# Kernel optimization log

Measured on AMD Instinct MI355X. Metric: run time of the kernel, lower is better.

## Reference

```python
import jax, jax.numpy as jnp
import numpy as np

D_MODEL = 1024
N_HEAD = 16
HEAD_DIM = D_MODEL // N_HEAD
B, T = 4, 1024
MIN_KEEP_H, MAX_KEEP_H = 2, 6


def setup_inputs() -> dict:
    key = jax.random.key(0)
    ks = jax.random.split(key, 8)
    x = jax.random.normal(ks[0], (B, T, D_MODEL), dtype=jnp.float32)
    # SignMaskLinear weight: uniform(-1, 1)
    q_w = jax.random.uniform(ks[1], (D_MODEL, D_MODEL), minval=-1.0, maxval=1.0, dtype=jnp.float32)
    # BitGhostLinear weights: randn
    k_w = jax.random.normal(ks[2], (D_MODEL, D_MODEL), dtype=jnp.float32)
    v_w = jax.random.normal(ks[3], (D_MODEL, D_MODEL), dtype=jnp.float32)
    o_w = jax.random.normal(ks[4], (D_MODEL, D_MODEL), dtype=jnp.float32)
    zeros = jnp.zeros((D_MODEL,), dtype=jnp.float32)
    return {"x": x, "q_w": q_w, "q_b": zeros, "k_w": k_w, "k_b": zeros,
            "v_w": v_w, "v_b": zeros, "o_w": o_w, "o_b": zeros}


def _ghost_attention(x, q_w, q_b, k_w, k_b, v_w, v_b, o_w, o_b):
    Bn, Tn, C = x.shape
    H, Dh = N_HEAD, HEAD_DIM
    # SignMaskLinear: effective weight is sign(w) * (w != 0)
    qw_eff = jnp.sign(q_w) * (q_w != 0).astype(x.dtype)
    q = (x @ qw_eff.T + q_b).reshape(Bn, Tn, H, Dh).transpose(0, 2, 1, 3)  # (B,H,T,Dh)
    k = (x @ k_w.T + k_b).reshape(Bn, Tn, H, Dh).transpose(0, 2, 1, 3)
    v = (x @ v_w.T + v_b).reshape(Bn, Tn, H, Dh).transpose(0, 2, 1, 3)
    # RMS-normalize q
    q = q / (jnp.sqrt(jnp.mean(q * q, axis=-1, keepdims=True)) + 1e-6)
    # Per-head top-k sparsification of q by |q| (static keep counts)
    ratios = np.linspace(0.35, 0.15, H)
    keep_counts = np.maximum((ratios * Dh).astype(np.int64), 1)  # trunc like .long()
    q_abs = jnp.abs(q)
    q_sorted = -jnp.sort(-q_abs, axis=-1)  # descending along Dh
    idx = jnp.asarray(keep_counts - 1, dtype=jnp.int32).reshape(1, H, 1, 1)
    thresh = jnp.take_along_axis(q_sorted, jnp.broadcast_to(idx, (Bn, H, Tn, 1)), axis=-1)
    q = q * (q_abs >= thresh).astype(q.dtype)
    # RMS-normalize k
    k = k / (jnp.sqrt(jnp.mean(k * k, axis=-1, keepdims=True)) + 1e-6)
    # Causal masked attention (no scale factor in original)
    logits = jnp.einsum('bhqd,bhkd->bhqk', q, k)
    causal = jnp.tril(jnp.ones((Tn, Tn), dtype=bool))
    logits = jnp.where(causal[None, None], logits, -jnp.inf)
    attn = jax.nn.softmax(logits, axis=-1)
    # Entropy-driven adaptive head pruning
    head_energy = jnp.mean(attn ** 2, axis=(2, 3))  # (B,H)
    head_prob = jax.nn.softmax(head_energy, axis=1)
    head_entropy = -jnp.sum(head_prob * jnp.log(head_prob + 1e-9), axis=1)  # (B,)
    ent_norm = jnp.clip(head_entropy / jnp.log(jnp.float32(H)), 0.0, 1.0)
    keep_h = jnp.round(MIN_KEEP_H + ent_norm * (MAX_KEEP_H - MIN_KEEP_H)).astype(jnp.int32)  # (B,)
    he_sorted = -jnp.sort(-head_energy, axis=1)  # descending (B,H)
    thresh_h = jnp.take_along_axis(he_sorted, (keep_h - 1)[:, None], axis=1)  # (B,1)
    head_mask = (head_energy >= thresh_h).astype(x.dtype)[:, :, None, None]  # (B,H,1,1)
    attn = attn * head_mask
    v = v * head_mask
    out = jnp.einsum('bhqk,bhkd->bhqd', attn, v).transpose(0, 2, 1, 3).reshape(Bn, Tn, C)
    return out @ o_w.T + o_b


def reference(x, q_w, q_b, k_w, k_b, v_w, v_b, o_w, o_b):
    return _ghost_attention(x, q_w, q_b, k_w, k_b, v_w, v_b, o_w, o_b)
```

## Files before the change

kernel.cpp:

```cpp
#include <hip/hip_runtime.h>
#include <math.h>

#define D_MODEL 1024
#define T_SEQ   1024
#define BATCH   4
#define NHEAD   16
#define HDIM    64

__constant__ int KEEPC[16] = {22,21,20,19,18,18,17,16,15,14,13,13,12,11,10,9};

typedef short bh8  __attribute__((ext_vector_type(8)));
typedef float f32x4 __attribute__((ext_vector_type(4)));
typedef int   i32x4 __attribute__((ext_vector_type(4)));

__device__ __forceinline__ unsigned short f2bf(float f) {
    unsigned int u = __float_as_uint(f);
    return (unsigned short)((u + 0x7FFFu + ((u >> 16) & 1u)) >> 16);
}
__device__ __forceinline__ float bf2f(unsigned short h) {
    return __uint_as_float(((unsigned int)h) << 16);
}

__global__ void cast_prep(const float* __restrict__ kw,
                          unsigned short* __restrict__ kwh,
                          unsigned short* __restrict__ kwl,
                          const float* __restrict__ vw,
                          unsigned short* __restrict__ vwb,
                          const float* __restrict__ ow,
                          unsigned short* __restrict__ owb,
                          const float* __restrict__ x,
                          signed char* __restrict__ dig,
                          const float* __restrict__ qw,
                          signed char* __restrict__ sg)
{
    const int NS = (D_MODEL * D_MODEL) / 8;
    const int NX = (BATCH * T_SEQ * D_MODEL) / 8;
    int i = blockIdx.x * 256 + threadIdx.x;

    if (i < 3 * NS) {
        const float* src; unsigned short* dh; unsigned short* dl = nullptr;
        long off;
        if (i < NS)          { src = kw; dh = kwh; dl = kwl; off = i; }
        else if (i < 2 * NS) { src = vw; dh = vwb; off = i - NS; }
        else                 { src = ow; dh = owb; off = i - 2 * NS; }
        long e = off * 8;
        alignas(16) float fl[8];
        *(float4*)&fl[0] = *(const float4*)(src + e);
        *(float4*)&fl[4] = *(const float4*)(src + e + 4);
        uint4 hp, lp;
        unsigned int* hpw = (unsigned int*)&hp;
        unsigned int* lpw = (unsigned int*)&lp;
        #pragma unroll
        for (int c = 0; c < 4; c++) {
            unsigned short h0 = f2bf(fl[2 * c]), h1 = f2bf(fl[2 * c + 1]);
            hpw[c] = (unsigned int)h0 | ((unsigned int)h1 << 16);
            if (dl) {
                unsigned short l0 = f2bf(fl[2 * c] - bf2f(h0));
                unsigned short l1 = f2bf(fl[2 * c + 1] - bf2f(h1));
                lpw[c] = (unsigned int)l0 | ((unsigned int)l1 << 16);
            }
        }
        *(uint4*)(dh + e) = hp;
        if (dl) *(uint4*)(dl + e) = lp;
    } else if (i < 3 * NS + NX) {
        long e = (long)(i - 3 * NS) * 8;
        alignas(16) float f[8];
        *(float4*)&f[0] = *(const float4*)(x + e);
        *(float4*)&f[4] = *(const float4*)(x + e + 4);
        signed char d[4][8];
        #pragma unroll
        for (int c = 0; c < 8; c++) {
            int n = (int)rintf(f[c] * 8388608.0f);
            int d0 = (signed char)(n & 0xff); n = (n - d0) >> 8;
            int d1 = (signed char)(n & 0xff); n = (n - d1) >> 8;
            int d2 = (signed char)(n & 0xff); n = (n - d2) >> 8;
            d[0][c] = (signed char)d0; d[1][c] = (signed char)d1;
            d[2][c] = (signed char)d2; d[3][c] = (signed char)n;
        }
        long row = e >> 10;
        int  kk  = (int)(e & 1023);
        long rt  = row >> 4;
        int  l15r = (int)(row & 15);
        int  kstep = kk >> 6;
        int  rg2 = (kk >> 4) & 3;
        int  L = rg2 * 16 + l15r;
        int  t = kk & 15;
        signed char* dp = dig + (rt << 16) + ((long)kstep << 12)
                              + ((long)L << 4) + t;
        #pragma unroll
        for (int p = 0; p < 4; p++)
            *(uint2*)(dp + (p << 10)) = *(uint2*)&d[p][0];
    } else if (i < 3 * NS + NX + NS) {
        long e = (long)(i - 3 * NS - NX) * 8;
        alignas(16) float f[8];
        *(float4*)&f[0] = *(const float4*)(qw + e);
        *(float4*)&f[4] = *(const float4*)(qw + e + 4);
        signed char s[8];
        #pragma unroll
        for (int c = 0; c < 8; c++)
            s[c] = (signed char)((f[c] > 0.f) - (f[c] < 0.f));
        long col = e >> 10;
        int  kk  = (int)(e & 1023);
        long ct  = col >> 4;
        int  l15c = (int)(col & 15);
        int  kstep = kk >> 6;
        int  rg2 = (kk >> 4) & 3;
        int  L = rg2 * 16 + l15c;
        int  t = kk & 15;
        signed char* sp = sg + (ct << 14) + ((long)kstep << 10)
                             + ((long)L << 4) + t;
        *(uint2*)sp = *(uint2*)&s[0];
    }
}

__global__ __launch_bounds__(256, 4) void gemm_q_i8(
    const signed char* __restrict__ dig, const signed char* __restrict__ sg,
    const float* __restrict__ Bi, unsigned short* __restrict__ Yq)
{
    int tid  = threadIdx.x;
    int blk  = blockIdx.x;
    int low  = blk & 7, rest = blk >> 3;
    int bn   = (rest & 15) * 64;
    int bm   = (((rest >> 4) << 3) + low) * 64;
    int wave = tid >> 6, lane = tid & 63;
    int l15  = lane & 15, rg = lane >> 4;

    int rt  = (bm >> 4) + wave;
    int ct0 = bn >> 4;

    i32x4 acc[4][4];
    #pragma unroll
    for (int p = 0; p < 4; p++)
        #pragma unroll
        for (int j = 0; j < 4; j++) acc[p][j] = (i32x4)0;

    const signed char* ar = dig + ((size_t)rt << 16) + (lane << 4);
    const signed char* br = sg + ((size_t)ct0 << 14) + (lane << 4);

    i32x4 aA[4], bA[4], aB[4], bB[4];
    #pragma unroll
    for (int p = 0; p < 4; p++) aA[p] = *(const i32x4*)(ar + (p << 10));
    #pragma unroll
    for (int j = 0; j < 4; j++) bA[j] = *(const i32x4*)(br + (j << 14));

    #pragma unroll
    for (int kk = 0; kk < 8; kk++) {
        #pragma unroll
        for (int p = 0; p < 4; p++) aB[p] = *(const i32x4*)(ar + 4096 + (p << 10));
        #pragma unroll
        for (int j = 0; j < 4; j++) bB[j] = *(const i32x4*)(br + 1024 + (j << 14));
        #pragma unroll
        for (int p = 0; p < 4; p++)
            #pragma unroll
            for (int j = 0; j < 4; j++)
                acc[p][j] = __builtin_amdgcn_mfma_i32_16x16x64_i8(
                    aA[p], bA[j], acc[p][j], 0, 0, 0);
        if (kk < 7) {
            #pragma unroll
            for (int p = 0; p < 4; p++) aA[p] = *(const i32x4*)(ar + 8192 + (p << 10));
            #pragma unroll
            for (int j = 0; j < 4; j++) bA[j] = *(const i32x4*)(br + 2048 + (j << 14));
        }
        #pragma unroll
        for (int p = 0; p < 4; p++)
            #pragma unroll
            for (int j = 0; j < 4; j++)
                acc[p][j] = __builtin_amdgcn_mfma_i32_16x16x64_i8(
                    aB[p], bB[j], acc[p][j], 0, 0, 0);
        ar += 8192; br += 2048;
    }

    int hh   = bn >> 6;
    int keep = KEEPC[hh];
    float bvj[4];
    #pragma unroll
    for (int j = 0; j < 4; j++) bvj[j] = Bi[bn + j * 16 + l15];

    float xv[4][4];
    #pragma unroll
    for (int j = 0; j < 4; j++)
        #pragma unroll
        for (int r = 0; r < 4; r++) {
            long t = (long)acc[0][j][r]
                   + ((long)acc[1][j][r] << 8)
                   + ((long)acc[2][j][r] << 16)
                   + ((long)acc[3][j][r] << 24);
            xv[j][r] = (float)((double)t * (1.0 / 8388608.0)) + bvj[j];
        }

    unsigned int shiftv = (unsigned int)(rg & 1) * 16;
    #pragma unroll
    for (int r = 0; r < 4; r++) {
        float ss = xv[0][r] * xv[0][r] + xv[1][r] * xv[1][r]
                 + xv[2][r] * xv[2][r] + xv[3][r] * xv[3][r];
        ss += __shfl_xor(ss, 1); ss += __shfl_xor(ss, 2);
        ss += __shfl_xor(ss, 4); ss += __shfl_xor(ss, 8);
        float rms = sqrtf(ss * (1.0f / 64.0f));

        float xn[4]; unsigned int ai[4];
        #pragma unroll
        for (int j = 0; j < 4; j++) {
            xn[j] = xv[j][r] / (rms + 1e-6f);
            ai[j] = __float_as_uint(fabsf(xn[j]));
        }

        unsigned int th = 0;
        for (int bit = 30; bit >= 0; --bit) {
            unsigned int cand = th | (1u << bit);
            int cnt = 0;
            #pragma unroll
            for (int j = 0; j < 4; j++) {
                unsigned long long bl = __ballot(ai[j] >= cand);
                unsigned int half = (rg & 2) ? (unsigned int)(bl >> 32)
                                             : (unsigned int)bl;
                cnt += __popc((half >> shiftv) & 0xFFFFu);
            }
            if (cnt >= keep) th = cand;
        }

        int row = bm + wave * 16 + rg * 4 + r;
        int bb = row >> 10, tt = row & 1023;
        unsigned int* qp32 = (unsigned int*)(Yq
            + (((size_t)(bb * NHEAD + hh)) * T_SEQ + tt) * 128);
        #pragma unroll
        for (int j = 0; j < 4; j++) {
            float o = (ai[j] < th) ? 0.f : xn[j];
            unsigned short hi = f2bf(o);
            unsigned short lo = f2bf(o - bf2f(hi));
            qp32[j * 16 + l15] = (unsigned int)hi | ((unsigned int)lo << 16);
        }
    }
}

#define GLDK 72

__global__ __launch_bounds__(256, 2) void gemm_kv(
    const float* __restrict__ A,
    const unsigned short* __restrict__ kwh, const unsigned short* __restrict__ kwl,
    const float* __restrict__ kb,
    const unsigned short* __restrict__ vwb, const float* __restrict__ vb,
    unsigned short* __restrict__ Yk, unsigned short* __restrict__ Yv)
{
    __shared__ unsigned short Ah[128 * GLDK];
    __shared__ unsigned short Al[128 * GLDK];
    __shared__ unsigned short Whs[128 * GLDK];
    __shared__ unsigned short Wls[128 * GLDK];

    int tid  = threadIdx.x;
    int blk  = blockIdx.x;
    int z    = blk >> 8;
    int split = (z == 0);
    int inner = blk & 255;
    int low  = inner & 7, rest = inner >> 3;
    int bn   = (rest & 7) * 128;
    int bm   = (((rest >> 3) << 3) + low) * 128;
    const unsigned short* Wh = split ? kwh : vwb;
    const unsigned short* Wl = split ? kwl : vwb;
    const float*          Bi = split ? kb : vb;

    int wave = tid >> 6, lane = tid & 63;
    int l15  = lane & 15, q4 = lane >> 4;
    int wm   = (wave >> 1) * 64, wn = (wave & 1) * 64;
    int srow = tid >> 1;
    int scol = (tid & 1) * 32;

    f32x4 acc[4][4];
    #pragma unroll
    for (int i = 0; i < 4; i++)
        #pragma unroll
        for (int j = 0; j < 4; j++) acc[i][j] = (f32x4)0.f;

    const float* ap = A + (size_t)(bm + srow) * D_MODEL + scol;
    const unsigned short* whp = Wh + (size_t)(bn + srow) * D_MODEL + scol;
    const unsigned short* wlp = Wl + (size_t)(bn + srow) * D_MODEL + scol;

    for (int k0 = 0; k0 < D_MODEL; k0 += 64) {
        alignas(16) float fl[32];
        #pragma unroll
        for (int c = 0; c < 8; c++) *(float4*)&fl[4 * c] = *(const float4*)(ap + 4 * c);
        uint4 w0 = *(const uint4*)(whp + 0),  w1 = *(const uint4*)(whp + 8);
        uint4 w2 = *(const uint4*)(whp + 16), w3 = *(const uint4*)(whp + 24);
        uint4 x0, x1, x2, x3;
        if (split) {
            x0 = *(const uint4*)(wlp + 0);  x1 = *(const uint4*)(wlp + 8);
            x2 = *(const uint4*)(wlp + 16); x3 = *(const uint4*)(wlp + 24);
        }
        ap += 64; whp += 64; wlp += 64;

        unsigned int hw[16], lw[16];
        #pragma unroll
        for (int c = 0; c < 16; c++) {
            unsigned short h0 = f2bf(fl[2 * c]), h1 = f2bf(fl[2 * c + 1]);
            hw[c] = (unsigned int)h0 | ((unsigned int)h1 << 16);
            if (split) {
                unsigned short l0 = f2bf(fl[2 * c] - bf2f(h0));
                unsigned short l1 = f2bf(fl[2 * c + 1] - bf2f(h1));
                lw[c] = (unsigned int)l0 | ((unsigned int)l1 << 16);
            }
        }

        __syncthreads();
        unsigned int* ah = (unsigned int*)&Ah[srow * GLDK + scol];
        #pragma unroll
        for (int g = 0; g < 4; g++)
            *(uint4*)(ah + 4 * g) = make_uint4(hw[4 * g], hw[4 * g + 1], hw[4 * g + 2], hw[4 * g + 3]);
        if (split) {
            unsigned int* al = (unsigned int*)&Al[srow * GLDK + scol];
            #pragma unroll
            for (int g = 0; g < 4; g++)
                *(uint4*)(al + 4 * g) = make_uint4(lw[4 * g], lw[4 * g + 1], lw[4 * g + 2], lw[4 * g + 3]);
        }
        unsigned short* ws = &Whs[srow * GLDK + scol];
        *(uint4*)(ws + 0) = w0; *(uint4*)(ws + 8)  = w1;
        *(uint4*)(ws + 16) = w2; *(uint4*)(ws + 24) = w3;
        if (split) {
            unsigned short* wl2 = &Wls[srow * GLDK + scol];
            *(uint4*)(wl2 + 0) = x0; *(uint4*)(wl2 + 8)  = x1;
            *(uint4*)(wl2 + 16) = x2; *(uint4*)(wl2 + 24) = x3;
        }
        __syncthreads();

        #pragma unroll
        for (int kc = 0; kc < 64; kc += 32) {
            bh8 ahf[4], whf[4];
            #pragma unroll
            for (int i = 0; i < 4; i++)
                ahf[i] = *(bh8*)&Ah[(wm + i * 16 + l15) * GLDK + kc + q4 * 8];
            #pragma unroll
            for (int j = 0; j < 4; j++)
                whf[j] = *(bh8*)&Whs[(wn + j * 16 + l15) * GLDK + kc + q4 * 8];
            #pragma unroll
            for (int i = 0; i < 4; i++)
                #pragma unroll
                for (int j = 0; j < 4; j++)
                    acc[i][j] = __builtin_amdgcn_mfma_f32_16x16x32_bf16(ahf[i], whf[j], acc[i][j], 0, 0, 0);
            if (split) {
                bh8 alf[4], wlf[4];
                #pragma unroll
                for (int i = 0; i < 4; i++)
                    alf[i] = *(bh8*)&Al[(wm + i * 16 + l15) * GLDK + kc + q4 * 8];
                #pragma unroll
                for (int j = 0; j < 4; j++)
                    wlf[j] = *(bh8*)&Wls[(wn + j * 16 + l15) * GLDK + kc + q4 * 8];
                #pragma unroll
                for (int i = 0; i < 4; i++)
                    #pragma unroll
                    for (int j = 0; j < 4; j++) {
                        acc[i][j] = __builtin_amdgcn_mfma_f32_16x16x32_bf16(ahf[i], wlf[j], acc[i][j], 0, 0, 0);
                        acc[i][j] = __builtin_amdgcn_mfma_f32_16x16x32_bf16(alf[i], whf[j], acc[i][j], 0, 0, 0);
                    }
            }
        }
    }

    if (split) {
        int hh = (bn + wn) >> 6;
        float bv[4];
        #pragma unroll
        for (int j = 0; j < 4; j++) bv[j] = Bi[bn + wn + j * 16 + l15];
        #pragma unroll
        for (int i = 0; i < 4; i++) {
            #pragma unroll
            for (int r = 0; r < 4; r++) {
                int row = bm + wm + i * 16 + q4 * 4 + r;
                int bb = row >> 10, tt = row & 1023;
                float vv[4]; float ss = 0.f;
                #pragma unroll
                for (int j = 0; j < 4; j++) {
                    vv[j] = acc[i][j][r] + bv[j];
                    ss += vv[j] * vv[j];
                }
                ss += __shfl_xor(ss, 1); ss += __shfl_xor(ss, 2);
                ss += __shfl_xor(ss, 4); ss += __shfl_xor(ss, 8);
                float rms = sqrtf(ss * (1.0f / 64.0f));
                unsigned short* kp = Yk + (((size_t)(bb * NHEAD + hh)) * T_SEQ + tt) * 128;
                #pragma unroll
                for (int j = 0; j < 4; j++) {
                    float xn = vv[j] / (rms + 1e-6f);
                    unsigned short hi = f2bf(xn);
                    unsigned short lo = f2bf(xn - bf2f(hi));
                    kp[j * 16 + l15]      = hi;
                    kp[64 + j * 16 + l15] = lo;
                }
            }
        }
    } else {
        #pragma unroll
        for (int j = 0; j < 4; j++) {
            int col = bn + wn + j * 16 + l15;
            int hh = col >> 6, dd = col & 63;
            float bvv = Bi[col];
            #pragma unroll
            for (int i = 0; i < 4; i++) {
                int row0 = bm + wm + i * 16 + q4 * 4;
                int bb = row0 >> 10, tt = row0 & 1023;
                uint2 u;
                u.x = (unsigned int)f2bf(acc[i][j][0] + bvv) | ((unsigned int)f2bf(acc[i][j][1] + bvv) << 16);
                u.y = (unsigned int)f2bf(acc[i][j][2] + bvv) | ((unsigned int)f2bf(acc[i][j][3] + bvv) << 16);
                *(uint2*)(Yv + ((size_t)(bb * NHEAD + hh) * HDIM + dd) * T_SEQ + tt) = u;
            }
        }
    }
}

#define KST 72

__global__ __launch_bounds__(256, 4) void attn_kernel(
    const unsigned short* __restrict__ Qsg,
    const unsigned short* __restrict__ Ksg,
    const unsigned short* __restrict__ Vtg,
    unsigned short* __restrict__ Ctx, double* __restrict__ He)
{
    __shared__ unsigned short Kh[64 * KST];
    __shared__ unsigned short Kl[64 * KST];
    __shared__ unsigned short Vt[64 * KST];
    __shared__ unsigned short Ps[4][16 * KST];

    int tid = threadIdx.x;
    int blk = blockIdx.x;
    int low = blk & 7, rest = blk >> 3;
    int qt  = 15 - (rest & 15);
    int r2  = rest >> 4;
    int h   = (r2 & 1) * 8 + low;
    int b   = r2 >> 1;
    int bh = b * NHEAD + h;
    size_t rbase = (size_t)bh * T_SEQ;

    int wave = tid >> 6, lane = tid & 63;
    int l15 = lane & 15, rg = lane >> 4;
    int srow = tid >> 2;
    int scol = (tid & 3) * 16;

    int qrow = qt * 64 + wave * 16 + l15;

    bh8 qf[2][2];
    {
        const unsigned int* qp32 = (const unsigned int*)(Qsg + (rbase + qrow) * 128);
        uint4 a = *(const uint4*)(qp32 + rg * 8);
        uint4 c = *(const uint4*)(qp32 + rg * 8 + 4);
        uint4 d = *(const uint4*)(qp32 + 32 + rg * 8);
        uint4 e = *(const uint4*)(qp32 + 32 + rg * 8 + 4);
        unsigned int hv[4], lv[4];
        hv[0] = __builtin_amdgcn_perm(a.y, a.x, 0x05040100u);
        hv[1] = __builtin_amdgcn_perm(a.w, a.z, 0x05040100u);
        hv[2] = __builtin_amdgcn_perm(c.y, c.x, 0x05040100u);
        hv[3] = __builtin_amdgcn_perm(c.w, c.z, 0x05040100u);
        lv[0] = __builtin_amdgcn_perm(a.y, a.x, 0x07060302u);
        lv[1] = __builtin_amdgcn_perm(a.w, a.z, 0x07060302u);
        lv[2] = __builtin_amdgcn_perm(c.y, c.x, 0x07060302u);
        lv[3] = __builtin_amdgcn_perm(c.w, c.z, 0x07060302u);
        qf[0][0] = *(bh8*)hv;
        qf[1][0] = *(bh8*)lv;
        hv[0] = __builtin_amdgcn_perm(d.y, d.x, 0x05040100u);
        hv[1] = __builtin_amdgcn_perm(d.w, d.z, 0x05040100u);
        hv[2] = __builtin_amdgcn_perm(e.y, e.x, 0x05040100u);
        hv[3] = __builtin_amdgcn_perm(e.w, e.z, 0x05040100u);
        lv[0] = __builtin_amdgcn_perm(d.y, d.x, 0x07060302u);
        lv[1] = __builtin_amdgcn_perm(d.w, d.z, 0x07060302u);
        lv[2] = __builtin_amdgcn_perm(e.y, e.x, 0x07060302u);
        lv[3] = __builtin_amdgcn_perm(e.w, e.z, 0x07060302u);
        qf[0][1] = *(bh8*)hv;
        qf[1][1] = *(bh8*)lv;
    }

    float m = -1e30f, l = 0.f, s2 = 0.f;
    f32x4 o[4];
    #pragma unroll
    for (int n = 0; n < 4; n++) o[n] = (f32x4)0.f;

    unsigned short* myPs = &Ps[wave][0];
    const unsigned short* vbase = Vtg + (size_t)bh * HDIM * T_SEQ;

    for (int kt = 0; kt <= qt; ++kt) {
        const unsigned short* krow = Ksg + (rbase + kt * 64 + srow) * 128;
        uint4 kh0 = *(const uint4*)(krow + scol);
        uint4 kh1 = *(const uint4*)(krow + scol + 8);
        uint4 kl0 = *(const uint4*)(krow + 64 + scol);
        uint4 kl1 = *(const uint4*)(krow + 64 + scol + 8);
        const unsigned short* vrow = vbase + (size_t)srow * T_SEQ + kt * 64 + scol;
        uint4 vv0 = *(const uint4*)(vrow);
        uint4 vv1 = *(const uint4*)(vrow + 8);

        __syncthreads();
        *(uint4*)&Kh[srow * KST + scol]     = kh0;
        *(uint4*)&Kh[srow * KST + scol + 8] = kh1;
        *(uint4*)&Kl[srow * KST + scol]     = kl0;
        *(uint4*)&Kl[srow * KST + scol + 8] = kl1;
        *(uint4*)&Vt[srow * KST + scol]     = vv0;
        *(uint4*)&Vt[srow * KST + scol + 8] = vv1;
        __syncthreads();

        f32x4 s[4];
        #pragma unroll
        for (int n = 0; n < 4; n++) s[n] = (f32x4)0.f;
        #pragma unroll
        for (int n = 0; n < 4; n++) {
            const unsigned short* kr = &Kh[(n * 16 + l15) * KST + rg * 8];
            const unsigned short* lr = &Kl[(n * 16 + l15) * KST + rg * 8];
            bh8 ah0 = *(const bh8*)(kr);
            bh8 ah1 = *(const bh8*)(kr + 32);
            bh8 al0 = *(const bh8*)(lr);
            bh8 al1 = *(const bh8*)(lr + 32);
            s[n] = __builtin_amdgcn_mfma_f32_16x16x32_bf16(ah0, qf[0][0], s[n], 0, 0, 0);
            s[n] = __builtin_amdgcn_mfma_f32_16x16x32_bf16(ah1, qf[0][1], s[n], 0, 0, 0);
            s[n] = __builtin_amdgcn_mfma_f32_16x16x32_bf16(ah0, qf[1][0], s[n], 0, 0, 0);
            s[n] = __builtin_amdgcn_mfma_f32_16x16x32_bf16(ah1, qf[1][1], s[n], 0, 0, 0);
            s[n] = __builtin_amdgcn_mfma_f32_16x16x32_bf16(al0, qf[0][0], s[n], 0, 0, 0);
            s[n] = __builtin_amdgcn_mfma_f32_16x16x32_bf16(al1, qf[0][1], s[n], 0, 0, 0);
        }

        if (kt == qt) {
            #pragma unroll
            for (int n = 0; n < 4; n++)
                #pragma unroll
                for (int e2 = 0; e2 < 4; e2++)
                    if (n * 16 + rg * 4 + e2 > wave * 16 + l15) s[n][e2] = -1e30f;
        }

        float mx = -1e30f;
        #pragma unroll
        for (int n = 0; n < 4; n++)
            #pragma unroll
            for (int e2 = 0; e2 < 4; e2++) mx = fmaxf(mx, s[n][e2]);
        mx = fmaxf(mx, __shfl_xor(mx, 16));
        mx = fmaxf(mx, __shfl_xor(mx, 32));
        float mn = fmaxf(m, mx);
        float alpha = __expf(m - mn);
        m = mn;
        float rs = 0.f, rs2 = 0.f;
        #pragma unroll
        for (int n = 0; n < 4; n++)
            #pragma unroll
            for (int e2 = 0; e2 < 4; e2++) {
                float pv = __expf(s[n][e2] - mn);
                s[n][e2] = pv;
                rs += pv; rs2 += pv * pv;
            }
        rs  += __shfl_xor(rs, 16);  rs  += __shfl_xor(rs, 32);
        rs2 += __shfl_xor(rs2, 16); rs2 += __shfl_xor(rs2, 32);
        l  = l * alpha + rs;
        s2 = s2 * alpha * alpha + rs2;

        #pragma unroll
        for (int n = 0; n < 4; n++) {
            uint2 u;
            u.x = (unsigned int)f2bf(s[n][0]) | ((unsigned int)f2bf(s[n][1]) << 16);
            u.y = (unsigned int)f2bf(s[n][2]) | ((unsigned int)f2bf(s[n][3]) << 16);
            *(uint2*)&myPs[l15 * KST + n * 16 + rg * 4] = u;
        }
        bh8 pf0 = *(bh8*)&myPs[l15 * KST + rg * 8];
        bh8 pf1 = *(bh8*)&myPs[l15 * KST + 32 + rg * 8];

        #pragma unroll
        for (int n = 0; n < 4; n++) {
            o[n] *= alpha;
            const unsigned short* vr = &Vt[(n * 16 + l15) * KST + rg * 8];
            bh8 v0 = *(const bh8*)(vr);
            bh8 v1 = *(const bh8*)(vr + 32);
            o[n] = __builtin_amdgcn_mfma_f32_16x16x32_bf16(v0, pf0, o[n], 0, 0, 0);
            o[n] = __builtin_amdgcn_mfma_f32_16x16x32_bf16(v1, pf1, o[n], 0, 0, 0);
        }
    }

    float linv = 1.f / l;
    float en = (rg == 0) ? s2 * linv * linv : 0.f;
    en += __shfl_xor(en, 1); en += __shfl_xor(en, 2);
    en += __shfl_xor(en, 4); en += __shfl_xor(en, 8);
    if (lane == 0) atomicAdd(&He[bh], (double)en);

    unsigned short* cp = Ctx + ((size_t)b * T_SEQ + qrow) * D_MODEL + h * HDIM;
    #pragma unroll
    for (int n = 0; n < 4; n++) {
        uint2 u;
        u.x = (unsigned int)f2bf(o[n][0] * linv) | ((unsigned int)f2bf(o[n][1] * linv) << 16);
        u.y = (unsigned int)f2bf(o[n][2] * linv) | ((unsigned int)f2bf(o[n][3] * linv) << 16);
        *(uint2*)(cp + n * 16 + rg * 4) = u;
    }
}

__global__ __launch_bounds__(256, 2) void gemm_obf(
    const unsigned short* __restrict__ A, const unsigned short* __restrict__ W,
    const float* __restrict__ Bi, float* __restrict__ Y,
    const double* __restrict__ He)
{
    __shared__ unsigned short As[128 * GLDK];
    __shared__ unsigned short Ws[128 * GLDK];
    __shared__ double hs[34];
    __shared__ float maskS[NHEAD];

    int tid  = threadIdx.x;
    int blk  = blockIdx.x;
    int low  = blk & 7, rest = blk >> 3;
    int bn   = (rest & 7) * 128;
    int bm   = (((rest >> 3) << 3) + low) * 128;
    int batch = bm >> 10;

    if (tid < NHEAD) hs[tid] = He[batch * NHEAD + tid] * (1.0 / (1024.0 * 1024.0));
    __syncthreads();
    if (tid < NHEAD) {
        double mx = hs[0];
        for (int h2 = 1; h2 < NHEAD; h2++) mx = fmax(mx, hs[h2]);
        hs[NHEAD + tid] = exp(hs[tid] - mx);
    }
    __syncthreads();
    if (tid == 0) {
        double s = 0.0;
        for (int h2 = 0; h2 < NHEAD; h2++) s += hs[NHEAD + h2];
        hs[32] = s;
    }
    __syncthreads();
    if (tid < NHEAD) {
        double ph = hs[NHEAD + tid] / hs[32];
        hs[NHEAD + tid] = ph * log(ph + 1e-9);
    }
    __syncthreads();
    if (tid == 0) {
        double ent = 0.0;
        for (int h2 = 0; h2 < NHEAD; h2++) ent -= hs[NHEAD + h2];
        double entn = ent / log(16.0);
        entn = fmin(fmax(entn, 0.0), 1.0);
        int keep = (int)rint(2.0 + entn * 4.0);
        if (keep < 1) keep = 1;
        if (keep > NHEAD) keep = NHEAD;
        double srt[NHEAD];
        for (int h2 = 0; h2 < NHEAD; h2++) srt[h2] = hs[h2];
        for (int i = 1; i < NHEAD; i++) {
            double v = srt[i]; int j = i - 1;
            while (j >= 0 && srt[j] < v) { srt[j + 1] = srt[j]; j--; }
            srt[j + 1] = v;
        }
        double th = srt[keep - 1];
        for (int h2 = 0; h2 < NHEAD; h2++)
            maskS[h2] = (hs[h2] >= th) ? 1.0f : 0.0f;
    }
    __syncthreads();

    int wave = tid >> 6, lane = tid & 63;
    int l15  = lane & 15, q4 = lane >> 4;
    int wm   = (wave >> 1) * 64, wn = (wave & 1) * 64;
    int srow = tid >> 1;
    int scol = (tid & 1) * 32;

    f32x4 acc[4][4];
    #pragma unroll
    for (int i = 0; i < 4; i++)
        #pragma unroll
        for (int j = 0; j < 4; j++) acc[i][j] = (f32x4)0.f;

    const unsigned short* ap = A + (size_t)(bm + srow) * D_MODEL + scol;
    const unsigned short* wp = W + (size_t)(bn + srow) * D_MODEL + scol;

    for (int k0 = 0; k0 < D_MODEL; k0 += 64) {
        if (maskS[k0 >> 6] == 0.f) { ap += 64; wp += 64; continue; }

        uint4 a0 = *(const uint4*)(ap + 0),  a1 = *(const uint4*)(ap + 8);
        uint4 a2 = *(const uint4*)(ap + 16), a3 = *(const uint4*)(ap + 24);
        uint4 w0 = *(const uint4*)(wp + 0),  w1 = *(const uint4*)(wp + 8);
        uint4 w2 = *(const uint4*)(wp + 16), w3 = *(const uint4*)(wp + 24);
        ap += 64; wp += 64;
        __syncthreads();
        unsigned short* as = &As[srow * GLDK + scol];
        *(uint4*)(as + 0) = a0; *(uint4*)(as + 8)  = a1;
        *(uint4*)(as + 16) = a2; *(uint4*)(as + 24) = a3;
        unsigned short* ws = &Ws[srow * GLDK + scol];
        *(uint4*)(ws + 0) = w0; *(uint4*)(ws + 8)  = w1;
        *(uint4*)(ws + 16) = w2; *(uint4*)(ws + 24) = w3;
        __syncthreads();

        #pragma unroll
        for (int kc = 0; kc < 64; kc += 32) {
            bh8 af[4], wf[4];
            #pragma unroll
            for (int i = 0; i < 4; i++)
                af[i] = *(bh8*)&As[(wm + i * 16 + l15) * GLDK + kc + q4 * 8];
            #pragma unroll
            for (int j = 0; j < 4; j++)
                wf[j] = *(bh8*)&Ws[(wn + j * 16 + l15) * GLDK + kc + q4 * 8];
            #pragma unroll
            for (int i = 0; i < 4; i++)
                #pragma unroll
                for (int j = 0; j < 4; j++)
                    acc[i][j] = __builtin_amdgcn_mfma_f32_16x16x32_bf16(af[i], wf[j], acc[i][j], 0, 0, 0);
        }
    }

    #pragma unroll
    for (int j = 0; j < 4; j++) {
        int col = bn + wn + j * 16 + l15;
        float bv = Bi[col];
        #pragma unroll
        for (int i = 0; i < 4; i++) {
            int row = bm + wm + i * 16 + q4 * 4;
            #pragma unroll
            for (int r = 0; r < 4; r++)
                Y[(size_t)(row + r) * D_MODEL + col] = acc[i][j][r] + bv;
        }
    }
}

extern "C" void kernel_launch(void* const* d_in, const int* in_sizes, int n_in,
                              void* d_out, int out_size, void* d_ws, size_t ws_size,
                              hipStream_t stream)
{
    (void)in_sizes; (void)n_in; (void)out_size; (void)ws_size;
    const float* x  = (const float*)d_in[0];
    const float* qw = (const float*)d_in[1];
    const float* qb = (const float*)d_in[2];
    const float* kw = (const float*)d_in[3];
    const float* kb = (const float*)d_in[4];
    const float* vw = (const float*)d_in[5];
    const float* vb = (const float*)d_in[6];
    const float* ow = (const float*)d_in[7];
    const float* ob = (const float*)d_in[8];
    float* out = (float*)d_out;

    char* base = (char*)d_ws;
    const size_t MB = (size_t)1024 * 1024;
    unsigned short* qbf  = (unsigned short*)(base);
    unsigned short* kbf  = (unsigned short*)(base + 16 * MB);
    unsigned short* vt   = (unsigned short*)(base + 32 * MB);
    unsigned short* ctxb = (unsigned short*)(base + 40 * MB);
    signed char*    dig  = (signed char*)(base + 32 * MB);
    unsigned short* kwh  = (unsigned short*)(base + 48 * MB);
    unsigned short* kwl  = (unsigned short*)(base + 50 * MB);
    unsigned short* vwb  = (unsigned short*)(base + 52 * MB);
    unsigned short* owb  = (unsigned short*)(base + 54 * MB);
    signed char*    sg   = (signed char*)(base + 56 * MB);
    double*         he   = (double*)(base + 57 * MB);

    hipMemsetAsync(he, 0, 64 * sizeof(double), stream);

    cast_prep<<<4096, 256, 0, stream>>>(kw, kwh, kwl, vw, vwb, ow, owb,
                                        x, dig, qw, sg);
    gemm_q_i8<<<1024, 256, 0, stream>>>(dig, sg, qb, qbf);
    gemm_kv<<<512, 256, 0, stream>>>(x, kwh, kwl, kb, vwb, vb, kbf, vt);
    attn_kernel<<<1024, 256, 0, stream>>>(qbf, kbf, vt, ctxb, he);
    gemm_obf<<<256, 256, 0, stream>>>(ctxb, owb, ob, out, he);
}
```

Baseline: 279.5 us.

## Precompute x bf16 hi/lo split in prep and prefetch next K-tile in gemm_kv

The cast_prep kernel now also writes bf16 hi and lo copies of x, so gemm_kv loads pre-split bf16 instead of fp32 and no longer redoes the split conversion in every tile block. gemm_kv also moves to register prefetching: the next K-slice's global loads are issued after the shared-memory store and before the MFMA compute. This is meant to remove redundant conversion ALU work and hide global load latency. It costs an extra 16MB write in prep plus more live registers, which may affect occupancy under launch_bounds(256,2).

Measured after the change: 256.3 us (median of 2 runs). 1.09x faster.

```diff
diff --git a/kernel.cpp b/kernel.cpp
--- a/kernel.cpp
+++ b/kernel.cpp
@@ -30,6 +30,8 @@
                           unsigned short* __restrict__ owb,
                           const float* __restrict__ x,
                           signed char* __restrict__ dig,
+                          unsigned short* __restrict__ xh,
+                          unsigned short* __restrict__ xl,
                           const float* __restrict__ qw,
                           signed char* __restrict__ sg)
 {
@@ -90,6 +92,19 @@
         #pragma unroll
         for (int p = 0; p < 4; p++)
             *(uint2*)(dp + (p << 10)) = *(uint2*)&d[p][0];
+        uint4 hp, lp;
+        unsigned int* hpw = (unsigned int*)&hp;
+        unsigned int* lpw = (unsigned int*)&lp;
+        #pragma unroll
+        for (int c = 0; c < 4; c++) {
+            unsigned short h0 = f2bf(f[2 * c]), h1 = f2bf(f[2 * c + 1]);
+            hpw[c] = (unsigned int)h0 | ((unsigned int)h1 << 16);
+            unsigned short l0 = f2bf(f[2 * c] - bf2f(h0));
+            unsigned short l1 = f2bf(f[2 * c + 1] - bf2f(h1));
+            lpw[c] = (unsigned int)l0 | ((unsigned int)l1 << 16);
+        }
+        *(uint4*)(xh + e) = hp;
+        *(uint4*)(xl + e) = lp;
     } else if (i < 3 * NS + NX + NS) {
         long e = (long)(i - 3 * NS - NX) * 8;
         alignas(16) float f[8];
@@ -235,7 +250,7 @@
 #define GLDK 72
 
 __global__ __launch_bounds__(256, 2) void gemm_kv(
-    const float* __restrict__ A,
+    const unsigned short* __restrict__ xhg, const unsigned short* __restrict__ xlg,
     const unsigned short* __restrict__ kwh, const unsigned short* __restrict__ kwl,
     const float* __restrict__ kb,
     const unsigned short* __restrict__ vwb, const float* __restrict__ vb,
@@ -270,55 +285,55 @@
         #pragma unroll
         for (int j = 0; j < 4; j++) acc[i][j] = (f32x4)0.f;
 
-    const float* ap = A + (size_t)(bm + srow) * D_MODEL + scol;
+    const unsigned short* ahp = xhg + (size_t)(bm + srow) * D_MODEL + scol;
+    const unsigned short* alp = xlg + (size_t)(bm + srow) * D_MODEL + scol;
     const unsigned short* whp = Wh + (size_t)(bn + srow) * D_MODEL + scol;
     const unsigned short* wlp = Wl + (size_t)(bn + srow) * D_MODEL + scol;
 
+    uint4 a0, a1, a2, a3, g0, g1, g2, g3;
+    uint4 w0, w1, w2, w3, x0, x1, x2, x3;
+    a0 = *(const uint4*)(ahp + 0);  a1 = *(const uint4*)(ahp + 8);
+    a2 = *(const uint4*)(ahp + 16); a3 = *(const uint4*)(ahp + 24);
+    w0 = *(const uint4*)(whp + 0);  w1 = *(const uint4*)(whp + 8);
+    w2 = *(const uint4*)(whp + 16); w3 = *(const uint4*)(whp + 24);
+    if (split) {
+        g0 = *(const uint4*)(alp + 0);  g1 = *(const uint4*)(alp + 8);
+        g2 = *(const uint4*)(alp + 16); g3 = *(const uint4*)(alp + 24);
+        x0 = *(const uint4*)(wlp + 0);  x1 = *(const uint4*)(wlp + 8);
+        x2 = *(const uint4*)(wlp + 16); x3 = *(const uint4*)(wlp + 24);
+    }
+
     for (int k0 = 0; k0 < D_MODEL; k0 += 64) {
-        alignas(16) float fl[32];
-        #pragma unroll
-        for (int c = 0; c < 8; c++) *(float4*)&fl[4 * c] = *(const float4*)(ap + 4 * c);
-        uint4 w0 = *(const uint4*)(whp + 0),  w1 = *(const uint4*)(whp + 8);
-        uint4 w2 = *(const uint4*)(whp + 16), w3 = *(const uint4*)(whp + 24);
-        uint4 x0, x1, x2, x3;
-        if (split) {
-            x0 = *(const uint4*)(wlp + 0);  x1 = *(const uint4*)(wlp + 8);
-            x2 = *(const uint4*)(wlp + 16); x3 = *(const uint4*)(wlp + 24);
-        }
-        ap += 64; whp += 64; wlp += 64;
-
-        unsigned int hw[16], lw[16];
-        #pragma unroll
-        for (int c = 0; c < 16; c++) {
-            unsigned short h0 = f2bf(fl[2 * c]), h1 = f2bf(fl[2 * c + 1]);
-            hw[c] = (unsigned int)h0 | ((unsigned int)h1 << 16);
-            if (split) {
-                unsigned short l0 = f2bf(fl[2 * c] - bf2f(h0));
-                unsigned short l1 = f2bf(fl[2 * c + 1] - bf2f(h1));
-                lw[c] = (unsigned int)l0 | ((unsigned int)l1 << 16);
-            }
-        }
-
         __syncthreads();
-        unsigned int* ah = (unsigned int*)&Ah[srow * GLDK + scol];
-        #pragma unroll
-        for (int g = 0; g < 4; g++)
-            *(uint4*)(ah + 4 * g) = make_uint4(hw[4 * g], hw[4 * g + 1], hw[4 * g + 2], hw[4 * g + 3]);
-        if (split) {
-            unsigned int* al = (unsigned int*)&Al[srow * GLDK + scol];
-            #pragma unroll
-            for (int g = 0; g < 4; g++)
-                *(uint4*)(al + 4 * g) = make_uint4(lw[4 * g], lw[4 * g + 1], lw[4 * g + 2], lw[4 * g + 3]);
-        }
+        unsigned short* as = &Ah[srow * GLDK + scol];
+        *(uint4*)(as + 0) = a0; *(uint4*)(as + 8)  = a1;
+        *(uint4*)(as + 16) = a2; *(uint4*)(as + 24) = a3;
         unsigned short* ws = &Whs[srow * GLDK + scol];
         *(uint4*)(ws + 0) = w0; *(uint4*)(ws + 8)  = w1;
         *(uint4*)(ws + 16) = w2; *(uint4*)(ws + 24) = w3;
         if (split) {
+            unsigned short* als = &Al[srow * GLDK + scol];
+            *(uint4*)(als + 0) = g0; *(uint4*)(als + 8)  = g1;
+            *(uint4*)(als + 16) = g2; *(uint4*)(als + 24) = g3;
             unsigned short* wl2 = &Wls[srow * GLDK + scol];
             *(uint4*)(wl2 + 0) = x0; *(uint4*)(wl2 + 8)  = x1;
             *(uint4*)(wl2 + 16) = x2; *(uint4*)(wl2 + 24) = x3;
         }
         __syncthreads();
+
+        if (k0 + 64 < D_MODEL) {
+            ahp += 64; alp += 64; whp += 64; wlp += 64;
+            a0 = *(const uint4*)(ahp + 0);  a1 = *(const uint4*)(ahp + 8);
+            a2 = *(const uint4*)(ahp + 16); a3 = *(const uint4*)(ahp + 24);
+            w0 = *(const uint4*)(whp + 0);  w1 = *(const uint4*)(whp + 8);
+            w2 = *(const uint4*)(whp + 16); w3 = *(const uint4*)(whp + 24);
+            if (split) {
+                g0 = *(const uint4*)(alp + 0);  g1 = *(const uint4*)(alp + 8);
+                g2 = *(const uint4*)(alp + 16); g3 = *(const uint4*)(alp + 24);
+                x0 = *(const uint4*)(wlp + 0);  x1 = *(const uint4*)(wlp + 8);
+                x2 = *(const uint4*)(wlp + 16); x3 = *(const uint4*)(wlp + 24);
+            }
+        }
 
         #pragma unroll
         for (int kc = 0; kc < 64; kc += 32) {
@@ -727,13 +742,15 @@
     unsigned short* owb  = (unsigned short*)(base + 54 * MB);
     signed char*    sg   = (signed char*)(base + 56 * MB);
     double*         he   = (double*)(base + 57 * MB);
+    unsigned short* xh   = (unsigned short*)(base + 58 * MB);
+    unsigned short* xl   = (unsigned short*)(base + 66 * MB);
 
     hipMemsetAsync(he, 0, 64 * sizeof(double), stream);
 
     cast_prep<<<4096, 256, 0, stream>>>(kw, kwh, kwl, vw, vwb, ow, owb,
-                                        x, dig, qw, sg);
+                                        x, dig, xh, xl, qw, sg);
     gemm_q_i8<<<1024, 256, 0, stream>>>(dig, sg, qb, qbf);
-    gemm_kv<<<512, 256, 0, stream>>>(x, kwh, kwl, kb, vwb, vb, kbf, vt);
+    gemm_kv<<<512, 256, 0, stream>>>(xh, xl, kwh, kwl, kb, vwb, vb, kbf, vt);
     attn_kernel<<<1024, 256, 0, stream>>>(qbf, kbf, vt, ctxb, he);
     gemm_obf<<<256, 256, 0, stream>>>(ctxb, owb, ob, out, he);
 }
```
